# Kernel tuning notes

Measured on AMD Instinct MI355X. Metric: run time of the kernel, lower is better.

Reference implementation:

```python
import jax, jax.numpy as jnp
import numpy as np

B, T1, T2, D, M = 64, 128, 160, 768, 64


def setup_inputs() -> dict:
    key = jax.random.key(0)
    k1, k2, k3 = jax.random.split(key, 3)
    v1 = jax.random.normal(k1, (B, T1, D), dtype=jnp.float32)
    v2 = jax.random.normal(k2, (B, T2, D), dtype=jnp.float32)
    # keras 'uniform' initializer: U(-0.05, 0.05); kernel logical shape (1,1,M,D) -> (M,D)
    kernel = jax.random.uniform(k3, (M, D), dtype=jnp.float32, minval=-0.05, maxval=0.05)
    return {"v1": v1, "v2": v2, "kernel": kernel}


def reference(v1, v2, kernel):
    # Original: expand v1 to [b,t1,1,m,d]*kernel, v2 to [b,1,t2,1,d],
    # numerator = sum_d(v1*v2), cosine_norm=False -> tanh(numerator).
    # Fused as a single einsum contraction over d (avoids [b,t1,t2,m,d] intermediate).
    num = jnp.einsum('bid,md,bjd->bijm', v1, kernel, v2)  # [b,t1,t2,m]
    return jnp.tanh(num)
```

## Files before the change

### kernel.cpp

```cpp
#include <hip/hip_runtime.h>
#include <hip/hip_bf16.h>

namespace {

constexpr int Bn = 64, T1 = 128, T2 = 160, D = 768, M = 64;
constexpr int NTOT = T2 * M;
constexpr int BM = 128;
constexpr int BN = 128;
constexpr int BK = 32;
constexpr int KSTEPS = D / BK;

typedef __bf16 bf16x8 __attribute__((ext_vector_type(8)));
typedef __bf16 bf16x4 __attribute__((ext_vector_type(4)));
typedef float  f32x4  __attribute__((ext_vector_type(4)));

__device__ __forceinline__ float fast_tanh(float x) {
  float e = __expf(2.0f * x);
  return 1.0f - 2.0f * __builtin_amdgcn_rcpf(e + 1.0f);
}

__global__ void cvt_bf16(const float* __restrict__ x, __bf16* __restrict__ y, int n4) {
  int i = blockIdx.x * blockDim.x + threadIdx.x;
  if (i < n4) {
    f32x4 v = ((const f32x4*)x)[i];
    bf16x4 o;
    o[0] = (__bf16)v.x; o[1] = (__bf16)v.y; o[2] = (__bf16)v.z; o[3] = (__bf16)v.w;
    ((bf16x4*)y)[i] = o;
  }
}

__device__ __forceinline__ void mul_bb2(uint4 a, uint4 b0, uint4 b1,
                                        bf16x8& r0, bf16x8& r1) {
  const unsigned hm = 0xffff0000u;
#define MPC_COMP(c, i0, i1)                                                   \
  {                                                                           \
    float al = __uint_as_float(a.c << 16), ah = __uint_as_float(a.c & hm);    \
    r0[i0] = (__bf16)(al * __uint_as_float(b0.c << 16));                      \
    r0[i1] = (__bf16)(ah * __uint_as_float(b0.c & hm));                       \
    r1[i0] = (__bf16)(al * __uint_as_float(b1.c << 16));                      \
    r1[i1] = (__bf16)(ah * __uint_as_float(b1.c & hm));                       \
  }
  MPC_COMP(x, 0, 1) MPC_COMP(y, 2, 3) MPC_COMP(z, 4, 5) MPC_COMP(w, 6, 7)
#undef MPC_COMP
}

__launch_bounds__(256, 5)
__global__ void mpcos_fast(const __bf16* __restrict__ v1b,
                           const __bf16* __restrict__ v2b,
                           const __bf16* __restrict__ kb,
                           float* __restrict__ out) {
  __shared__ __bf16 Al[2][BM * BK];
  __shared__ __bf16 Bl[2][BN * BK];

  const int t    = threadIdx.x;
  const int lane = t & 63;
  const int w    = t >> 6;
  const int bjm  = blockIdx.x;
  const int bb   = blockIdx.y;

  const int sm = t >> 2, sc = t & 3;
  const __bf16* kp   = kb + sm * D + sc * 8;
  const __bf16* v2p0 = v2b + ((size_t)(bb * T2 + bjm * 2)) * D + sc * 8;
  const __bf16* v2p1 = v2p0 + D;
  const int boff = sm * BK + ((sc ^ ((sm >> 1) & 3)) * 8);

  const int arow = w * 32 + (lane >> 2);
  const int achk = (lane & 3) ^ ((lane >> 3) & 3);
  const __bf16* av1 = v1b + ((size_t)bb * T1 + arow) * D + achk * 8;
  const int adst = (w * 32) * BK;

  const int wrow = (w & 1) * 64;
  const int wcol = (w >> 1) * 64;
  const int lr = lane & 15, lg = lane >> 4;
  const int swc = (lg ^ ((lr >> 1) & 3)) * 8;

  f32x4 acc[4][4] = {};

  {
#pragma unroll
    for (int q = 0; q < 2; ++q)
      __builtin_amdgcn_global_load_lds(
          (const __attribute__((address_space(1))) void*)(av1 + q * 16 * D),
          (__attribute__((address_space(3))) void*)&Al[0][adst + q * 16 * BK],
          16, 0, 0);
    uint4 k0 = *(const uint4*)kp;
    uint4 u0 = *(const uint4*)v2p0;
    uint4 u1 = *(const uint4*)v2p1;
    bf16x8 r0, r1;
    mul_bb2(k0, u0, u1, r0, r1);
    *(bf16x8*)&Bl[0][boff]           = r0;
    *(bf16x8*)&Bl[0][64 * BK + boff] = r1;
    __syncthreads();
  }

  int cur = 0;
  for (int ks = 0; ks < KSTEPS; ++ks) {
    const int nxt = cur ^ 1;
    const bool more = (ks + 1 < KSTEPS);
    uint4 pk, pu0, pu1;
    if (more) {
      const int ko = (ks + 1) * BK;
#pragma unroll
      for (int q = 0; q < 2; ++q)
        __builtin_amdgcn_global_load_lds(
            (const __attribute__((address_space(1))) void*)(av1 + ko + q * 16 * D),
            (__attribute__((address_space(3))) void*)&Al[nxt][adst + q * 16 * BK],
            16, 0, 0);
      pk  = *(const uint4*)(kp + ko);
      pu0 = *(const uint4*)(v2p0 + ko);
      pu1 = *(const uint4*)(v2p1 + ko);
    }

    bf16x8 af[4], bfr[4];
#pragma unroll
    for (int ii = 0; ii < 4; ++ii)
      af[ii] = *(const bf16x8*)&Al[cur][(wrow + ii * 16 + lr) * BK + swc];
#pragma unroll
    for (int jj = 0; jj < 4; ++jj)
      bfr[jj] = *(const bf16x8*)&Bl[cur][(wcol + jj * 16 + lr) * BK + swc];
#pragma unroll
    for (int jj = 0; jj < 4; ++jj)
#pragma unroll
      for (int ii = 0; ii < 4; ++ii)
        acc[jj][ii] = __builtin_amdgcn_mfma_f32_16x16x32_bf16(
            bfr[jj], af[ii], acc[jj][ii], 0, 0, 0);

    if (more) {
      bf16x8 r0, r1;
      mul_bb2(pk, pu0, pu1, r0, r1);
      *(bf16x8*)&Bl[nxt][boff]           = r0;
      *(bf16x8*)&Bl[nxt][64 * BK + boff] = r1;
      __syncthreads();
    }
    cur = nxt;
  }

  float* obase = out + (size_t)bb * T1 * NTOT + (size_t)bjm * BN;
#pragma unroll
  for (int jj = 0; jj < 4; ++jj) {
#pragma unroll
    for (int ii = 0; ii < 4; ++ii) {
      const int row = wrow + ii * 16 + lr;
      const int col = wcol + jj * 16 + lg * 4;
      f32x4 v;
#pragma unroll
      for (int r = 0; r < 4; ++r) v[r] = fast_tanh(acc[jj][ii][r]);
      *(f32x4*)&obase[(size_t)row * NTOT + col] = v;
    }
  }
}

__launch_bounds__(256, 3)
__global__ void mpcos_ref(const float* __restrict__ v1f,
                          const float* __restrict__ v2,
                          const float* __restrict__ kern,
                          float* __restrict__ out) {
  constexpr int BKr = 64;
  __shared__ __bf16 Alds[BM * BKr];
  __shared__ __bf16 Blds[BN * BKr];

  const int t = threadIdx.x, lane = t & 63, w = t >> 6;
  const int bjm = blockIdx.x, bb = blockIdx.y;
  const int srow = t >> 1, sc4 = (t & 1) * 4;
  const int sm = srow & (M - 1), sj = srow >> 6, ssw = srow & 7;
  const float* kp  = kern + sm * D + sc4 * 8;
  const float* v2p = v2 + ((size_t)(bb * T2 + bjm * 2 + sj)) * D + sc4 * 8;
  const float* v1p = v1f + ((size_t)bb * T1 + srow) * D + sc4 * 8;
  const int wrow = (w & 1) * 64, wcol = (w >> 1) * 64;
  const int lr = lane & 15, lg = lane >> 4, lr7 = lr & 7;

  f32x4 acc[4][4] = {};
  for (int ks = 0; ks < D / BKr; ++ks) {
    const int kb = ks * BKr;
    __syncthreads();
    const f32x4* a4 = (const f32x4*)(v1p + kb);
#pragma unroll
    for (int q = 0; q < 4; ++q) {
      f32x4 x0 = a4[2 * q], x1 = a4[2 * q + 1];
      bf16x8 wv;
      wv[0] = (__bf16)x0.x; wv[1] = (__bf16)x0.y; wv[2] = (__bf16)x0.z; wv[3] = (__bf16)x0.w;
      wv[4] = (__bf16)x1.x; wv[5] = (__bf16)x1.y; wv[6] = (__bf16)x1.z; wv[7] = (__bf16)x1.w;
      *(bf16x8*)&Alds[srow * BKr + (((sc4 + q) ^ ssw) * 8)] = wv;
    }
    const f32x4* k4 = (const f32x4*)(kp + kb);
    const f32x4* u4 = (const f32x4*)(v2p + kb);
#pragma unroll
    for (int q = 0; q < 4; ++q) {
      f32x4 a0 = k4[2 * q], a1 = k4[2 * q + 1];
      f32x4 b0 = u4[2 * q], b1 = u4[2 * q + 1];
      bf16x8 wv;
      wv[0] = (__bf16)(a0.x * b0.x); wv[1] = (__bf16)(a0.y * b0.y);
      wv[2] = (__bf16)(a0.z * b0.z); wv[3] = (__bf16)(a0.w * b0.w);
      wv[4] = (__bf16)(a1.x * b1.x); wv[5] = (__bf16)(a1.y * b1.y);
      wv[6] = (__bf16)(a1.z * b1.z); wv[7] = (__bf16)(a1.w * b1.w);
      *(bf16x8*)&Blds[srow * BKr + (((sc4 + q) ^ ssw) * 8)] = wv;
    }
    __syncthreads();
#pragma unroll
    for (int kk = 0; kk < BKr; kk += 32) {
      const int cb = kk >> 3;
      const int st = (((cb + lg) ^ lr7) * 8);
      bf16x8 af[4], bfr[4];
#pragma unroll
      for (int ii = 0; ii < 4; ++ii)
        af[ii] = *(const bf16x8*)&Alds[(wrow + ii * 16 + lr) * BKr + st];
#pragma unroll
      for (int jj = 0; jj < 4; ++jj)
        bfr[jj] = *(const bf16x8*)&Blds[(wcol + jj * 16 + lr) * BKr + st];
#pragma unroll
      for (int ii = 0; ii < 4; ++ii)
#pragma unroll
        for (int jj = 0; jj < 4; ++jj)
          acc[ii][jj] = __builtin_amdgcn_mfma_f32_16x16x32_bf16(
              af[ii], bfr[jj], acc[ii][jj], 0, 0, 0);
    }
  }
  float* obase = out + (size_t)bb * T1 * NTOT + (size_t)bjm * BN;
#pragma unroll
  for (int ii = 0; ii < 4; ++ii)
#pragma unroll
    for (int r = 0; r < 4; ++r) {
      const int row = wrow + ii * 16 + lg * 4 + r;
      float* orow = obase + (size_t)row * NTOT + wcol + lr;
#pragma unroll
      for (int jj = 0; jj < 4; ++jj)
        orow[jj * 16] = fast_tanh(acc[ii][jj][r]);
    }
}

}

extern "C" void kernel_launch(void* const* d_in, const int* in_sizes, int n_in,
                              void* d_out, int out_size, void* d_ws, size_t ws_size,
                              hipStream_t stream) {
  const float* v1   = (const float*)d_in[0];
  const float* v2   = (const float*)d_in[1];
  const float* kern = (const float*)d_in[2];
  float* out = (float*)d_out;

  const size_t n_v1 = (size_t)Bn * T1 * D;
  const size_t n_v2 = (size_t)Bn * T2 * D;
  const size_t n_k  = (size_t)M * D;
  const size_t off_v2 = n_v1 * 2;
  const size_t off_k  = off_v2 + n_v2 * 2;
  const size_t need   = off_k + n_k * 2;

  if (ws_size >= need) {
    __bf16* v1b = (__bf16*)((char*)d_ws);
    __bf16* v2b = (__bf16*)((char*)d_ws + off_v2);
    __bf16* kb  = (__bf16*)((char*)d_ws + off_k);
    cvt_bf16<<<(int)(n_v1 / 4 / 256), 256, 0, stream>>>(v1, v1b, (int)(n_v1 / 4));
    cvt_bf16<<<(int)(n_v2 / 4 / 256), 256, 0, stream>>>(v2, v2b, (int)(n_v2 / 4));
    cvt_bf16<<<(int)(n_k  / 4 / 256), 256, 0, stream>>>(kern, kb, (int)(n_k / 4));
    mpcos_fast<<<dim3(NTOT / BN, Bn), 256, 0, stream>>>(v1b, v2b, kb, out);
  } else {
    mpcos_ref<<<dim3(NTOT / BN, Bn), 256, 0, stream>>>(v1, v2, kern, out);
  }
}
```

Measured before the change: 579.3 us.

## Widen fast kernel tile to 256 columns with 512 threads and batch-grouped block order

The fast GEMM kernel now covers a 128x256 output tile with 8 waves instead of 128x128 with 4, so each loaded v1 tile serves twice as many output columns. The workgroup index is also remapped so that eight consecutive workgroups cover eight different batches at the same column block, meant to share the kernel-matrix rows in cache. The aim is to cut global and LDS traffic per output. In exchange each block uses more LDS and registers, and the grid has half as many workgroups, which may lower occupancy.

```diff
diff --git a/kernel.cpp b/kernel.cpp
--- a/kernel.cpp
+++ b/kernel.cpp
@@ -6,9 +6,11 @@
 constexpr int Bn = 64, T1 = 128, T2 = 160, D = 768, M = 64;
 constexpr int NTOT = T2 * M;
 constexpr int BM = 128;
-constexpr int BN = 128;
+constexpr int BN = 256;
 constexpr int BK = 32;
 constexpr int KSTEPS = D / BK;
+constexpr int NBJM = NTOT / BN;
+constexpr int NWG  = NBJM * Bn;
 
 typedef __bf16 bf16x8 __attribute__((ext_vector_type(8)));
 typedef __bf16 bf16x4 __attribute__((ext_vector_type(4)));
@@ -44,7 +46,7 @@
 #undef MPC_COMP
 }
 
-__launch_bounds__(256, 5)
+__launch_bounds__(512, 4)
 __global__ void mpcos_fast(const __bf16* __restrict__ v1b,
                            const __bf16* __restrict__ v2b,
                            const __bf16* __restrict__ kb,
@@ -55,19 +57,24 @@
   const int t    = threadIdx.x;
   const int lane = t & 63;
   const int w    = t >> 6;
-  const int bjm  = blockIdx.x;
-  const int bb   = blockIdx.y;
-
-  const int sm = t >> 2, sc = t & 3;
-  const __bf16* kp   = kb + sm * D + sc * 8;
-  const __bf16* v2p0 = v2b + ((size_t)(bb * T2 + bjm * 2)) * D + sc * 8;
-  const __bf16* v2p1 = v2p0 + D;
-  const int boff = sm * BK + ((sc ^ ((sm >> 1) & 3)) * 8);
-
-  const int arow = w * 32 + (lane >> 2);
+
+  const int flat = blockIdx.y * NBJM + blockIdx.x;
+  const int r    = flat >> 3;
+  const int bjm  = r % NBJM;
+  const int bb   = (flat & 7) + 8 * (r / NBJM);
+
+  const int smi = t >> 3, sc = t & 3, sjh = (t >> 2) & 1;
+  const __bf16* kp   = kb + smi * D + sc * 8;
+  const __bf16* v2pa = v2b + ((size_t)(bb * T2 + bjm * 4 + sjh)) * D + sc * 8;
+  const __bf16* v2pb = v2pa + 2 * D;
+  const int swz    = (sc ^ ((smi >> 1) & 3)) * 8;
+  const int boff_a = (sjh * 64 + smi) * BK + swz;
+  const int boff_b = ((sjh + 2) * 64 + smi) * BK + swz;
+
+  const int arow = w * 16 + (lane >> 2);
   const int achk = (lane & 3) ^ ((lane >> 3) & 3);
   const __bf16* av1 = v1b + ((size_t)bb * T1 + arow) * D + achk * 8;
-  const int adst = (w * 32) * BK;
+  const int adst = w * 16 * BK;
 
   const int wrow = (w & 1) * 64;
   const int wcol = (w >> 1) * 64;
@@ -77,19 +84,16 @@
   f32x4 acc[4][4] = {};
 
   {
-#pragma unroll
-    for (int q = 0; q < 2; ++q)
-      __builtin_amdgcn_global_load_lds(
-          (const __attribute__((address_space(1))) void*)(av1 + q * 16 * D),
-          (__attribute__((address_space(3))) void*)&Al[0][adst + q * 16 * BK],
-          16, 0, 0);
+    __builtin_amdgcn_global_load_lds(
+        (const __attribute__((address_space(1))) void*)av1,
+        (__attribute__((address_space(3))) void*)&Al[0][adst], 16, 0, 0);
     uint4 k0 = *(const uint4*)kp;
-    uint4 u0 = *(const uint4*)v2p0;
-    uint4 u1 = *(const uint4*)v2p1;
+    uint4 u0 = *(const uint4*)v2pa;
+    uint4 u1 = *(const uint4*)v2pb;
     bf16x8 r0, r1;
     mul_bb2(k0, u0, u1, r0, r1);
-    *(bf16x8*)&Bl[0][boff]           = r0;
-    *(bf16x8*)&Bl[0][64 * BK + boff] = r1;
+    *(bf16x8*)&Bl[0][boff_a] = r0;
+    *(bf16x8*)&Bl[0][boff_b] = r1;
     __syncthreads();
   }
 
@@ -100,15 +104,12 @@
     uint4 pk, pu0, pu1;
     if (more) {
       const int ko = (ks + 1) * BK;
-#pragma unroll
-      for (int q = 0; q < 2; ++q)
-        __builtin_amdgcn_global_load_lds(
-            (const __attribute__((address_space(1))) void*)(av1 + ko + q * 16 * D),
-            (__attribute__((address_space(3))) void*)&Al[nxt][adst + q * 16 * BK],
-            16, 0, 0);
+      __builtin_amdgcn_global_load_lds(
+          (const __attribute__((address_space(1))) void*)(av1 + ko),
+          (__attribute__((address_space(3))) void*)&Al[nxt][adst], 16, 0, 0);
       pk  = *(const uint4*)(kp + ko);
-      pu0 = *(const uint4*)(v2p0 + ko);
-      pu1 = *(const uint4*)(v2p1 + ko);
+      pu0 = *(const uint4*)(v2pa + ko);
+      pu1 = *(const uint4*)(v2pb + ko);
     }
 
     bf16x8 af[4], bfr[4];
@@ -128,8 +129,8 @@
     if (more) {
       bf16x8 r0, r1;
       mul_bb2(pk, pu0, pu1, r0, r1);
-      *(bf16x8*)&Bl[nxt][boff]           = r0;
-      *(bf16x8*)&Bl[nxt][64 * BK + boff] = r1;
+      *(bf16x8*)&Bl[nxt][boff_a] = r0;
+      *(bf16x8*)&Bl[nxt][boff_b] = r1;
       __syncthreads();
     }
     cur = nxt;
@@ -144,7 +145,7 @@
       const int col = wcol + jj * 16 + lg * 4;
       f32x4 v;
 #pragma unroll
-      for (int r = 0; r < 4; ++r) v[r] = fast_tanh(acc[jj][ii][r]);
+      for (int r2 = 0; r2 < 4; ++r2) v[r2] = fast_tanh(acc[jj][ii][r2]);
       *(f32x4*)&obase[(size_t)row * NTOT + col] = v;
     }
   }
@@ -155,9 +156,10 @@
                           const float* __restrict__ v2,
                           const float* __restrict__ kern,
                           float* __restrict__ out) {
+  constexpr int BNr = 128;
   constexpr int BKr = 64;
   __shared__ __bf16 Alds[BM * BKr];
-  __shared__ __bf16 Blds[BN * BKr];
+  __shared__ __bf16 Blds[BNr * BKr];
 
   const int t = threadIdx.x, lane = t & 63, w = t >> 6;
   const int bjm = blockIdx.x, bb = blockIdx.y;
@@ -215,7 +217,7 @@
               af[ii], bfr[jj], acc[ii][jj], 0, 0, 0);
     }
   }
-  float* obase = out + (size_t)bb * T1 * NTOT + (size_t)bjm * BN;
+  float* obase = out + (size_t)bb * T1 * NTOT + (size_t)bjm * BNr;
 #pragma unroll
   for (int ii = 0; ii < 4; ++ii)
 #pragma unroll
@@ -252,8 +254,8 @@
     cvt_bf16<<<(int)(n_v1 / 4 / 256), 256, 0, stream>>>(v1, v1b, (int)(n_v1 / 4));
     cvt_bf16<<<(int)(n_v2 / 4 / 256), 256, 0, stream>>>(v2, v2b, (int)(n_v2 / 4));
     cvt_bf16<<<(int)(n_k  / 4 / 256), 256, 0, stream>>>(kern, kb, (int)(n_k / 4));
-    mpcos_fast<<<dim3(NTOT / BN, Bn), 256, 0, stream>>>(v1b, v2b, kb, out);
+    mpcos_fast<<<dim3(NBJM, Bn), 512, 0, stream>>>(v1b, v2b, kb, out);
   } else {
-    mpcos_ref<<<dim3(NTOT / BN, Bn), 256, 0, stream>>>(v1, v2, kern, out);
-  }
-}
+    mpcos_ref<<<dim3(NTOT / 128, Bn), 256, 0, stream>>>(v1, v2, kern, out);
+  }
+}
```

Result: faster. 513.4 us (-11.4%).
